# Optimization experiments

Measured on AMD Instinct MI355X. Metric: run time of the kernel, lower is better.

Reference implementation:

```python
import jax, jax.numpy as jnp
import numpy as np

SPEED_OF_SOUND = 343.0
SAMPLING_FREQUENCY = 96000.0
CROP_LENGTH = 256


def setup_inputs() -> dict:
    key = jax.random.key(0)
    k1, k2, k3, k4 = jax.random.split(key, 4)
    B1, B2, R, T = 4, 1024, 64, 16384
    recordings = jax.random.normal(k1, (B1, R, T), dtype=jnp.float32)
    sample_locations = jax.random.uniform(k2, (B1, B2, 3), dtype=jnp.float32)  # points in unit cube
    emitter_location = jnp.array([0.0, 0.0, 0.5], dtype=jnp.float32)
    receiver_locations = jax.random.uniform(k3, (R, 3), dtype=jnp.float32) * 0.2
    canonical_echo = jax.random.normal(k4, (CROP_LENGTH,), dtype=jnp.float32)
    return {
        "recordings": recordings,
        "sample_locations": sample_locations,
        "emitter_location": emitter_location,
        "receiver_locations": receiver_locations,
        "canonical_echo": canonical_echo,
    }


def _time_of_flight_crop(recordings, sample_locations, emitter_location, receiver_locations):
    # recordings: (B1, R, T); sample_locations: (B1, B2, 3)
    B1, R, T = recordings.shape
    # emitter -> sample distance: (B1, B2)
    d_es = jnp.linalg.norm(sample_locations - emitter_location, axis=-1)
    # sample -> receiver distance: (B1, B2, R)
    d_sr = jnp.linalg.norm(
        sample_locations[:, :, None, :] - receiver_locations[None, None, :, :], axis=-1
    )
    # fractional start sample index of the echo window: (B1, B2, R)
    start = (d_es[:, :, None] + d_sr) / SPEED_OF_SOUND * SAMPLING_FREQUENCY
    # fractional sample indices for the crop window: (B1, B2, R, L)
    idx = start[..., None] + jnp.arange(CROP_LENGTH, dtype=recordings.dtype)
    i0f = jnp.floor(idx)
    frac = idx - i0f
    i0 = jnp.clip(i0f.astype(jnp.int32), 0, T - 1)
    i1 = jnp.clip(i0 + 1, 0, T - 1)
    # gather per (B1, R) row: vmap over B2 so we never broadcast recordings to (B1,B2,R,T)
    gather = jax.vmap(
        lambda i: jnp.take_along_axis(recordings, i, axis=-1), in_axes=1, out_axes=1
    )
    v0 = gather(i0)  # (B1, B2, R, L)
    v1 = gather(i1)
    return v0 * (1.0 - frac) + v1 * frac  # linear interpolation


def reference(recordings, sample_locations, emitter_location, receiver_locations, canonical_echo):
    cropped = _time_of_flight_crop(
        recordings, sample_locations, emitter_location, receiver_locations
    )  # (B1, B2, R, L)
    # dot with canonical echo template over L, clamp at 0, sum over receivers
    products = jnp.einsum("bqrl,l->bqr", cropped, canonical_echo)
    products = jnp.maximum(products, 0.0)
    magnitude = jnp.sum(products, axis=2)  # (B1, B2)
    return magnitude
```

## Files before the change

### kernel.cpp

```cpp
#include <hip/hip_runtime.h>

#define T_LEN 16384
#define R_CNT 64
#define CROP 256
#define B2_CNT 1024
#define COPY_DW 1164

typedef float f4 __attribute__((ext_vector_type(4), aligned(16)));

__global__ void zero_out(float* __restrict__ out) {
    out[blockIdx.x * 256 + threadIdx.x] = 0.0f;
}

__global__ __launch_bounds__(256) void tof_kernel(
    const float* __restrict__ recordings,
    const float* __restrict__ sample_locations,
    const float* __restrict__ emitter,
    const float* __restrict__ receivers,
    const float* __restrict__ echo,
    float* __restrict__ out)
{
    const int blk  = blockIdx.x;
    const int b1   = blk >> 8;
    const int r    = (blk >> 2) & 63;
    const int qc   = blk & 3;
    const int tid  = threadIdx.x;
    const int lane = tid & 63;
    const int wave = tid >> 6;
    const int i16  = lane & 15;
    const int grp  = lane >> 4;

    __shared__ __align__(16) float s_copy[4 * COPY_DW];
    __shared__ __align__(16) float s_echo[CROP];
    __shared__ __align__(16) float s_echo_sh[CROP + 4];
    __shared__ float2 s_sf[256];

    {
        const float ev = echo[tid];
        s_echo[tid] = ev;
        s_echo_sh[tid + 1] = ev;
        if (tid == 0) s_echo_sh[0] = 0.0f;
    }

    const float* __restrict__ row = recordings + ((size_t)b1 * R_CNT + r) * T_LEN;
    #pragma unroll
    for (int c = 0; c < 4; ++c)
        for (int j = tid; j < COPY_DW; j += 256)
            s_copy[c * COPY_DW + j] = row[j + c];

    {
        const int q = qc * 256 + tid;
        const float sx = sample_locations[(b1 * B2_CNT + q) * 3 + 0];
        const float sy = sample_locations[(b1 * B2_CNT + q) * 3 + 1];
        const float sz = sample_locations[(b1 * B2_CNT + q) * 3 + 2];
        const float ex = emitter[0], ey = emitter[1], ez = emitter[2];
        const float dex = sx - ex, dey = sy - ey, dez = sz - ez;
        const float d_es = sqrtf(fmaf(dex, dex, fmaf(dey, dey, dez * dez)));
        const float rx = receivers[r * 3 + 0];
        const float ry = receivers[r * 3 + 1];
        const float rz = receivers[r * 3 + 2];
        const float dx = sx - rx, dy = sy - ry, dz = sz - rz;
        const float d_sr = sqrtf(fmaf(dx, dx, fmaf(dy, dy, dz * dz)));

        const float SCALE = 96000.0f / 343.0f;
        const float start = (d_es + d_sr) * SCALE;
        const float i0f   = floorf(start);
        int s0 = (int)i0f;
        s0 = s0 < 0 ? 0 : (s0 > 904 ? 904 : s0);
        s_sf[tid] = make_float2(__int_as_float(s0), start - i0f);
    }
    __syncthreads();

    f4 e[4], ep[4];
    #pragma unroll
    for (int cc = 0; cc < 4; ++cc) {
        e[cc]  = *reinterpret_cast<const f4*>(&s_echo[cc * 64 + i16 * 4]);
        ep[cc] = *reinterpret_cast<const f4*>(&s_echo_sh[cc * 64 + i16 * 4]);
    }
    const float e_last = s_echo[CROP - 1];

    #pragma unroll 4
    for (int pass = 0; pass < 16; ++pass) {
        const int q_local = wave * 64 + pass * 4 + grp;
        const float2 sf   = s_sf[q_local];
        const int   s0    = __float_as_int(sf.x);
        const float frac  = sf.y;
        const int   c     = s0 & 3;
        const int   bdw   = s0 >> 2;

        const float* pb = &s_copy[c * COPY_DW + 4 * (bdw + i16)];

        float A = 0.0f, Bt = 0.0f;
        #pragma unroll
        for (int cc = 0; cc < 4; ++cc) {
            const f4 v = *reinterpret_cast<const f4*>(pb + cc * 64);
            A  = fmaf(e[cc][0],  v[0], fmaf(e[cc][1],  v[1], fmaf(e[cc][2],  v[2], fmaf(e[cc][3],  v[3], A))));
            Bt = fmaf(ep[cc][0], v[0], fmaf(ep[cc][1], v[1], fmaf(ep[cc][2], v[2], fmaf(ep[cc][3], v[3], Bt))));
        }
        const float v256 = s_copy[c * COPY_DW + 4 * bdw + 256];
        Bt = fmaf(e_last, (i16 == 15) ? v256 : 0.0f, Bt);

        float pr = fmaf(frac, Bt - A, A);
        pr += __shfl_xor(pr, 1);
        pr += __shfl_xor(pr, 2);
        pr += __shfl_xor(pr, 4);
        pr += __shfl_xor(pr, 8);

        if (i16 == 0) {
            const int q = qc * 256 + q_local;
            atomicAdd(&out[b1 * B2_CNT + q], fmaxf(pr, 0.0f));
        }
    }
}

extern "C" void kernel_launch(void* const* d_in, const int* in_sizes, int n_in,
                              void* d_out, int out_size, void* d_ws, size_t ws_size,
                              hipStream_t stream) {
    const float* recordings       = (const float*)d_in[0];
    const float* sample_locations = (const float*)d_in[1];
    const float* emitter          = (const float*)d_in[2];
    const float* receivers        = (const float*)d_in[3];
    const float* echo             = (const float*)d_in[4];
    float* out                    = (float*)d_out;

    const int B1 = in_sizes[1] / (B2_CNT * 3);

    zero_out<<<dim3(B1 * B2_CNT / 256), dim3(256), 0, stream>>>(out);
    tof_kernel<<<dim3(B1 * R_CNT * 4), dim3(256), 0, stream>>>(
        recordings, sample_locations, emitter, receivers, echo, out);
}
```

Measured before the change: 81.03 us.

## Pack recordings and echo to fp16 and use dot2 with finer query split

```diff
diff --git a/kernel.cpp b/kernel.cpp
--- a/kernel.cpp
+++ b/kernel.cpp
@@ -4,15 +4,32 @@
 #define R_CNT 64
 #define CROP 256
 #define B2_CNT 1024
-#define COPY_DW 1164
+#define QS 128
+#define CDW 584
+#define CDW_S 656
 
-typedef float f4 __attribute__((ext_vector_type(4), aligned(16)));
+typedef _Float16 h2 __attribute__((ext_vector_type(2)));
+
+__device__ __forceinline__ h2 as_h2(unsigned u) {
+    union { unsigned u; h2 h; } v; v.u = u; return v.h;
+}
+
+#if __has_builtin(__builtin_amdgcn_fdot2)
+__device__ __forceinline__ float DOT2(unsigned a, unsigned b, float c) {
+    return __builtin_amdgcn_fdot2(as_h2(a), as_h2(b), c, false);
+}
+#else
+__device__ __forceinline__ float DOT2(unsigned a, unsigned b, float c) {
+    h2 x = as_h2(a), y = as_h2(b);
+    return fmaf((float)x[0], (float)y[0], fmaf((float)x[1], (float)y[1], c));
+}
+#endif
 
 __global__ void zero_out(float* __restrict__ out) {
     out[blockIdx.x * 256 + threadIdx.x] = 0.0f;
 }
 
-__global__ __launch_bounds__(256) void tof_kernel(
+__global__ __launch_bounds__(256, 6) void tof_kernel(
     const float* __restrict__ recordings,
     const float* __restrict__ sample_locations,
     const float* __restrict__ emitter,
@@ -21,35 +38,35 @@
     float* __restrict__ out)
 {
     const int blk  = blockIdx.x;
-    const int b1   = blk >> 8;
-    const int r    = (blk >> 2) & 63;
-    const int qc   = blk & 3;
+    const int b1   = blk >> 9;
+    const int r    = (blk >> 3) & 63;
+    const int qc   = blk & 7;
     const int tid  = threadIdx.x;
     const int lane = tid & 63;
     const int wave = tid >> 6;
-    const int i16  = lane & 15;
-    const int grp  = lane >> 4;
+    const int i8   = lane & 7;
+    const int g3   = lane >> 3;
 
-    __shared__ __align__(16) float s_copy[4 * COPY_DW];
-    __shared__ __align__(16) float s_echo[CROP];
-    __shared__ __align__(16) float s_echo_sh[CROP + 4];
-    __shared__ float2 s_sf[256];
-
-    {
-        const float ev = echo[tid];
-        s_echo[tid] = ev;
-        s_echo_sh[tid + 1] = ev;
-        if (tid == 0) s_echo_sh[0] = 0.0f;
-    }
+    __shared__ unsigned s_copy[8 * CDW_S];
+    __shared__ unsigned s_echo_pk[CROP / 2];
+    __shared__ float2   s_sf[QS];
 
     const float* __restrict__ row = recordings + ((size_t)b1 * R_CNT + r) * T_LEN;
     #pragma unroll
-    for (int c = 0; c < 4; ++c)
-        for (int j = tid; j < COPY_DW; j += 256)
-            s_copy[c * COPY_DW + j] = row[j + c];
+    for (int c = 0; c < 8; ++c)
+        for (int j = tid; j < CDW; j += 256) {
+            const float a = row[c + 2 * j];
+            const float b = row[c + 2 * j + 1];
+            s_copy[c * CDW_S + j + 4 * (j >> 5)] =
+                __builtin_bit_cast(unsigned, __builtin_amdgcn_cvt_pkrtz(a, b));
+        }
 
-    {
-        const int q = qc * 256 + tid;
+    if (tid < CROP / 2)
+        s_echo_pk[tid] = __builtin_bit_cast(unsigned,
+            __builtin_amdgcn_cvt_pkrtz(echo[2 * tid], echo[2 * tid + 1]));
+
+    if (tid < QS) {
+        const int q = qc * QS + tid;
         const float sx = sample_locations[(b1 * B2_CNT + q) * 3 + 0];
         const float sy = sample_locations[(b1 * B2_CNT + q) * 3 + 1];
         const float sz = sample_locations[(b1 * B2_CNT + q) * 3 + 2];
@@ -71,45 +88,47 @@
     }
     __syncthreads();
 
-    f4 e[4], ep[4];
+    unsigned e[16];
     #pragma unroll
-    for (int cc = 0; cc < 4; ++cc) {
-        e[cc]  = *reinterpret_cast<const f4*>(&s_echo[cc * 64 + i16 * 4]);
-        ep[cc] = *reinterpret_cast<const f4*>(&s_echo_sh[cc * 64 + i16 * 4]);
-    }
-    const float e_last = s_echo[CROP - 1];
+    for (int n = 0; n < 4; ++n)
+        *(uint4*)&e[4 * n] = *(const uint4*)&s_echo_pk[i8 * 16 + 4 * n];
 
-    #pragma unroll 4
-    for (int pass = 0; pass < 16; ++pass) {
-        const int q_local = wave * 64 + pass * 4 + grp;
-        const float2 sf   = s_sf[q_local];
-        const int   s0    = __float_as_int(sf.x);
-        const float frac  = sf.y;
-        const int   c     = s0 & 3;
-        const int   bdw   = s0 >> 2;
+    for (int pass = 0; pass < 4; ++pass) {
+        const int ql = wave * 32 + pass * 8 + g3;
+        const float2 sf  = s_sf[ql];
+        const int   s0   = __float_as_int(sf.x);
+        const float frac = sf.y;
+        const int   c    = s0 & 7;
+        const int   D    = 4 * (s0 >> 3) + 16 * i8;
 
-        const float* pb = &s_copy[c * COPY_DW + 4 * (bdw + i16)];
+        const unsigned* __restrict__ cb = &s_copy[c * CDW_S];
 
-        float A = 0.0f, Bt = 0.0f;
+        unsigned d[17];
         #pragma unroll
-        for (int cc = 0; cc < 4; ++cc) {
-            const f4 v = *reinterpret_cast<const f4*>(pb + cc * 64);
-            A  = fmaf(e[cc][0],  v[0], fmaf(e[cc][1],  v[1], fmaf(e[cc][2],  v[2], fmaf(e[cc][3],  v[3], A))));
-            Bt = fmaf(ep[cc][0], v[0], fmaf(ep[cc][1], v[1], fmaf(ep[cc][2], v[2], fmaf(ep[cc][3], v[3], Bt))));
+        for (int n = 0; n < 4; ++n) {
+            const int dj = D + 4 * n;
+            *(uint4*)&d[4 * n] = *(const uint4*)&cb[dj + 4 * (dj >> 5)];
         }
-        const float v256 = s_copy[c * COPY_DW + 4 * bdw + 256];
-        Bt = fmaf(e_last, (i16 == 15) ? v256 : 0.0f, Bt);
+        {
+            const int dj = D + 16;
+            d[16] = cb[dj + 4 * (dj >> 5)];
+        }
 
-        float pr = fmaf(frac, Bt - A, A);
+        float A = 0.0f, B = 0.0f;
+        #pragma unroll
+        for (int k = 0; k < 16; ++k) {
+            A = DOT2(e[k], d[k], A);
+            const unsigned sh = (d[k] >> 16) | (d[k + 1] << 16);
+            B = DOT2(e[k], sh, B);
+        }
+
+        float pr = fmaf(frac, B - A, A);
         pr += __shfl_xor(pr, 1);
         pr += __shfl_xor(pr, 2);
         pr += __shfl_xor(pr, 4);
-        pr += __shfl_xor(pr, 8);
 
-        if (i16 == 0) {
-            const int q = qc * 256 + q_local;
-            atomicAdd(&out[b1 * B2_CNT + q], fmaxf(pr, 0.0f));
-        }
+        if (i8 == 0)
+            atomicAdd(&out[b1 * B2_CNT + qc * QS + ql], fmaxf(pr, 0.0f));
     }
 }
 
@@ -126,6 +145,6 @@
     const int B1 = in_sizes[1] / (B2_CNT * 3);
 
     zero_out<<<dim3(B1 * B2_CNT / 256), dim3(256), 0, stream>>>(out);
-    tof_kernel<<<dim3(B1 * R_CNT * 4), dim3(256), 0, stream>>>(
+    tof_kernel<<<dim3(B1 * R_CNT * 8), dim3(256), 0, stream>>>(
         recordings, sample_locations, emitter, receivers, echo, out);
 }
```

Result: slower. 84.54 us (+4.3%).
